# Performance work log

Hardware: AMD Instinct MI355X
Metric: run time of the kernel (lower is better)

## Reference

```python
import jax, jax.numpy as jnp
import numpy as np

EPS = 1e-08


def setup_inputs() -> dict:
    key = jax.random.key(0)
    x = jax.random.normal(key, (16384, 1024), dtype=jnp.float32)
    return {"x": x}


def reference(x) -> jnp.ndarray:
    # L2-normalize rows (torch F.normalize clamps the norm by eps=1e-12)
    norm = jnp.maximum(jnp.linalg.norm(x, axis=-1, keepdims=True), 1e-12)
    xn = x / norm
    # B x B cosine similarity
    sim = xn @ xn.T
    # exclude self-similarity on the diagonal
    B = sim.shape[0]
    diag = jnp.eye(B, dtype=bool)
    sim = jnp.where(diag, -jnp.inf, sim)
    max_sim = jnp.max(sim, axis=1)
    # squared L2 distance to nearest neighbor on the unit sphere
    distances = jnp.sqrt(2.0 - 2.0 * max_sim + EPS)
    return -jnp.mean(jnp.log(distances))
```

## Files before the change

kernel.cpp:

```cpp
#include <hip/hip_runtime.h>
#include <hip/hip_bf16.h>

#define NROWS 16384
#define DIM   1024
#define NT    8
#define NTILE 128
#define NBLK  (NTILE * (NTILE + 1) / 2)
#define SW    16

typedef int i32x4 __attribute__((ext_vector_type(4)));

__device__ __forceinline__ unsigned fkey(float f) {
    unsigned u = __float_as_uint(f);
    return (u & 0x80000000u) ? ~u : (u | 0x80000000u);
}
__device__ __forceinline__ float funkey(unsigned k) {
    unsigned u = (k & 0x80000000u) ? (k & 0x7fffffffu) : ~k;
    return __uint_as_float(u);
}

__global__ void normalize_rows(const float* __restrict__ x,
                               signed char* __restrict__ xq,
                               float* __restrict__ sinv,
                               unsigned* __restrict__ rowmax) {
    const int row = blockIdx.x;
    const int t = threadIdx.x;
    const float4 v = ((const float4*)(x + (size_t)row * DIM))[t];
    float ss = v.x * v.x + v.y * v.y + v.z * v.z + v.w * v.w;
#pragma unroll
    for (int off = 32; off > 0; off >>= 1) ss += __shfl_xor(ss, off);
    __shared__ float wss[4];
    __shared__ int   wqs[4];
    if ((t & 63) == 0) wss[t >> 6] = ss;
    __syncthreads();
    const float tot = wss[0] + wss[1] + wss[2] + wss[3];
    const float scale = 127.0f / fmaxf(sqrtf(tot), 1e-12f);
    int qx = __float2int_rn(v.x * scale);
    int qy = __float2int_rn(v.y * scale);
    int qz = __float2int_rn(v.z * scale);
    int qw = __float2int_rn(v.w * scale);
    qx = max(-127, min(127, qx)); qy = max(-127, min(127, qy));
    qz = max(-127, min(127, qz)); qw = max(-127, min(127, qw));
    const int p = (qx & 0xff) | ((qy & 0xff) << 8) | ((qz & 0xff) << 16) | ((qw & 0xff) << 24);
    ((int*)(xq + (size_t)row * DIM))[t] = p;
    int qs = qx * qx + qy * qy + qz * qz + qw * qw;
#pragma unroll
    for (int off = 32; off > 0; off >>= 1) qs += __shfl_xor(qs, off);
    if ((t & 63) == 0) wqs[t >> 6] = qs;
    __syncthreads();
    if (t == 0) {
        const int qtot = max(wqs[0] + wqs[1] + wqs[2] + wqs[3], 1);
        sinv[row] = 1.0f / sqrtf((float)qtot);
        rowmax[row] = 0u;
    }
}


#define SB() __builtin_amdgcn_sched_barrier(0)

__global__ __launch_bounds__(256, 2)
void simmax_kernel(const signed char* __restrict__ xq,
                   const float* __restrict__ sinv,
                   unsigned* __restrict__ rowmax) {
    const int bid = blockIdx.x;
    int rem = (bid & 7) * (NBLK / 8) + (bid >> 3);
    int s = 0;
    for (;;) {
        const int sz = 256 * s + 136;
        if (rem < sz) break;
        rem -= sz;
        ++s;
    }
    int it, jt;
    const int full = 256 * s;
    if (rem < full) {
        it = rem >> 4;
        jt = SW * s + (rem & 15);
    } else {
        int r2 = rem - full;
        int d = 0;
        while (r2 >= SW - d) { r2 -= SW - d; ++d; }
        it = SW * s + d;
        jt = it + r2;
    }
    const bool diag = (jt == it);
    const int rowBase = it * 128;
    const int colBase = jt * 128;

    __shared__ __align__(16) char lds[2][2][128][128];
    __shared__ unsigned redmax[256];

    const int t    = threadIdx.x;
    const int lane = t & 63;
    const int wid  = t >> 6;
    const int wr2  = wid >> 1;
    const int wc2  = wid & 1;
    const int l15  = lane & 15;
    const int hi   = lane >> 4;

    redmax[t] = 0u;

    const signed char* srcp[8];
#pragma unroll
    for (int j = 0; j < 8; ++j) {
        const int c   = j * 256 + t;
        const int op  = c >> 10;
        const int cc  = c & 1023;
        const int row = cc >> 3;
        const int ch  = cc & 7;
        const int gr  = (op ? colBase : rowBase) + row;
        srcp[j] = xq + (size_t)gr * DIM + (ch ^ (row & 7)) * 16;
    }

#pragma unroll
    for (int j = 0; j < 8; ++j) {
        __builtin_amdgcn_global_load_lds(
            (const __attribute__((address_space(1))) void*)srcp[j],
            (__attribute__((address_space(3))) void*)(&lds[0][0][0][0] + (j * 256 + wid * 64) * 16),
            16, 0, 0);
        srcp[j] += 128;
    }
    asm volatile("s_waitcnt vmcnt(0)" ::: "memory");
    __builtin_amdgcn_s_barrier();
    SB();

    i32x4 acc[4][4];
#pragma unroll
    for (int m = 0; m < 4; ++m)
#pragma unroll
        for (int n = 0; n < 4; ++n)
            acc[m][n] = (i32x4){0, 0, 0, 0};

    for (int tk = 0; tk < NT; ++tk) {
        char* curb = &lds[tk & 1][0][0][0];
        char* nxtb = &lds[(tk & 1) ^ 1][0][0][0];
        const bool pf = (tk + 1 < NT);

        i32x4 af[4][2], bf[4][2];
#pragma unroll
        for (int m = 0; m < 4; ++m)
#pragma unroll
            for (int kk = 0; kk < 2; ++kk) {
                const int row = wr2 * 64 + m * 16 + l15;
                const int chn = (kk * 4 + hi) ^ (row & 7);
                af[m][kk] = *(const i32x4*)(curb + row * 128 + chn * 16);
            }
        if (pf) {
#pragma unroll
            for (int j = 0; j < 4; ++j) {
                __builtin_amdgcn_global_load_lds(
                    (const __attribute__((address_space(1))) void*)srcp[j],
                    (__attribute__((address_space(3))) void*)(nxtb + (j * 256 + wid * 64) * 16),
                    16, 0, 0);
                srcp[j] += 128;
            }
        }
#pragma unroll
        for (int n = 0; n < 4; ++n)
#pragma unroll
            for (int kk = 0; kk < 2; ++kk) {
                const int row = wc2 * 64 + n * 16 + l15;
                const int chn = (kk * 4 + hi) ^ (row & 7);
                bf[n][kk] = *(const i32x4*)(curb + 16384 + row * 128 + chn * 16);
            }
        if (pf) {
#pragma unroll
            for (int j = 4; j < 8; ++j) {
                __builtin_amdgcn_global_load_lds(
                    (const __attribute__((address_space(1))) void*)srcp[j],
                    (__attribute__((address_space(3))) void*)(nxtb + (j * 256 + wid * 64) * 16),
                    16, 0, 0);
                srcp[j] += 128;
            }
        }
        __builtin_amdgcn_s_setprio(1);
#pragma unroll
        for (int m = 0; m < 4; ++m)
#pragma unroll
            for (int n = 0; n < 4; ++n)
#pragma unroll
                for (int kk = 0; kk < 2; ++kk)
                    acc[m][n] = __builtin_amdgcn_mfma_i32_16x16x64_i8(
                        af[m][kk], bf[n][kk], acc[m][n], 0, 0, 0);
        __builtin_amdgcn_s_setprio(0);

        asm volatile("s_waitcnt vmcnt(0)" ::: "memory");
        __builtin_amdgcn_s_barrier();
        SB();
    }

    const int g  = lane >> 4;
    const int cl = lane & 15;

    float scl_col[4];
#pragma unroll
    for (int n = 0; n < 4; ++n)
        scl_col[n] = sinv[colBase + wc2 * 64 + n * 16 + cl];
    float srow[4][4];
#pragma unroll
    for (int m = 0; m < 4; ++m)
#pragma unroll
        for (int r = 0; r < 4; ++r)
            srow[m][r] = sinv[rowBase + wr2 * 64 + m * 16 + g * 4 + r];

#pragma unroll
    for (int m = 0; m < 4; ++m)
#pragma unroll
        for (int r = 0; r < 4; ++r) {
            const int grow = wr2 * 64 + m * 16 + g * 4 + r;
            float v = -1e30f;
#pragma unroll
            for (int n = 0; n < 4; ++n) {
                const int gcol = wc2 * 64 + n * 16 + cl;
                float f = (float)acc[m][n][r] * scl_col[n];
                if (diag && grow == gcol) f = -1e30f;
                v = fmaxf(v, f);
            }
            v = fmaxf(v, __shfl_xor(v, 1));
            v = fmaxf(v, __shfl_xor(v, 2));
            v = fmaxf(v, __shfl_xor(v, 4));
            v = fmaxf(v, __shfl_xor(v, 8));
            if (cl == 0) atomicMax(&redmax[grow], fkey(v));
        }

    if (!diag) {
#pragma unroll
        for (int n = 0; n < 4; ++n) {
            float v = -1e30f;
#pragma unroll
            for (int m = 0; m < 4; ++m)
#pragma unroll
                for (int r = 0; r < 4; ++r)
                    v = fmaxf(v, (float)acc[m][n][r] * srow[m][r]);
            v = fmaxf(v, __shfl_xor(v, 16));
            v = fmaxf(v, __shfl_xor(v, 32));
            if (g == 0) atomicMax(&redmax[128 + wc2 * 64 + n * 16 + cl], fkey(v));
        }
    }
    __syncthreads();

    const unsigned k = redmax[t];
    if (t < 128) {
        atomicMax(rowmax + rowBase + t, k);
    } else if (!diag) {
        atomicMax(rowmax + colBase + (t - 128), k);
    }
}

__global__ void finalize_kernel(const unsigned* __restrict__ rowmax,
                                const float* __restrict__ sinv,
                                float* __restrict__ out) {
    const int t = threadIdx.x;
    float s = 0.f;
    for (int r = t; r < NROWS; r += 256) {
        const float m = fminf(sinv[r] * funkey(rowmax[r]), 1.0f);
        s += logf(2.0f - 2.0f * m + 1e-8f);
    }
#pragma unroll
    for (int off = 32; off > 0; off >>= 1) s += __shfl_xor(s, off);
    __shared__ float ws[4];
    if ((t & 63) == 0) ws[t >> 6] = s;
    __syncthreads();
    if (t == 0) out[0] = -0.5f * (ws[0] + ws[1] + ws[2] + ws[3]) / (float)NROWS;
}

extern "C" void kernel_launch(void* const* d_in, const int* in_sizes, int n_in,
                              void* d_out, int out_size, void* d_ws, size_t ws_size,
                              hipStream_t stream) {
    const float* x = (const float*)d_in[0];
    signed char* xq = (signed char*)d_ws;
    float* sinv = (float*)((char*)d_ws + (size_t)NROWS * DIM);
    unsigned* rowmax = (unsigned*)((char*)d_ws + (size_t)NROWS * DIM + NROWS * sizeof(float));
    float* out = (float*)d_out;

    normalize_rows<<<NROWS, 256, 0, stream>>>(x, xq, sinv, rowmax);
    simmax_kernel<<<NBLK, 256, 0, stream>>>(xq, sinv, rowmax);
    finalize_kernel<<<1, 256, 0, stream>>>(rowmax, sinv, out);
}
```

Before: 256.8 us.

## Load B operand directly from global into registers, halve LDS, raise occupancy

The B (column) tile is no longer staged through LDS. Each lane reads its MFMA B fragments straight from global memory, while only the A tile stays double-buffered in LDS. This halves LDS use per block, and launch bounds are raised to allow 4 blocks per CU, aiming to cut LDS traffic and improve latency hiding. The risk is that the direct B loads are uncoalesced, unswizzled and not prefetched, so MFMA may stall on global latency.

```diff
diff --git a/kernel.cpp b/kernel.cpp
--- a/kernel.cpp
+++ b/kernel.cpp
@@ -58,7 +58,7 @@
 
 #define SB() __builtin_amdgcn_sched_barrier(0)
 
-__global__ __launch_bounds__(256, 2)
+__global__ __launch_bounds__(256, 4)
 void simmax_kernel(const signed char* __restrict__ xq,
                    const float* __restrict__ sinv,
                    unsigned* __restrict__ rowmax) {
@@ -87,7 +87,7 @@
     const int rowBase = it * 128;
     const int colBase = jt * 128;
 
-    __shared__ __align__(16) char lds[2][2][128][128];
+    __shared__ __align__(16) char ldsA[2][16384];
     __shared__ unsigned redmax[256];
 
     const int t    = threadIdx.x;
@@ -100,25 +100,27 @@
 
     redmax[t] = 0u;
 
-    const signed char* srcp[8];
-#pragma unroll
-    for (int j = 0; j < 8; ++j) {
+    const signed char* srcA[4];
+#pragma unroll
+    for (int j = 0; j < 4; ++j) {
         const int c   = j * 256 + t;
-        const int op  = c >> 10;
-        const int cc  = c & 1023;
-        const int row = cc >> 3;
-        const int ch  = cc & 7;
-        const int gr  = (op ? colBase : rowBase) + row;
-        srcp[j] = xq + (size_t)gr * DIM + (ch ^ (row & 7)) * 16;
-    }
-
-#pragma unroll
-    for (int j = 0; j < 8; ++j) {
+        const int row = c >> 3;
+        const int ch  = c & 7;
+        srcA[j] = xq + (size_t)(rowBase + row) * DIM + (ch ^ (row & 7)) * 16;
+    }
+
+    const signed char* bn[4];
+#pragma unroll
+    for (int n = 0; n < 4; ++n)
+        bn[n] = xq + (size_t)(colBase + wc2 * 64 + n * 16 + l15) * DIM + hi * 16;
+
+#pragma unroll
+    for (int j = 0; j < 4; ++j) {
         __builtin_amdgcn_global_load_lds(
-            (const __attribute__((address_space(1))) void*)srcp[j],
-            (__attribute__((address_space(3))) void*)(&lds[0][0][0][0] + (j * 256 + wid * 64) * 16),
+            (const __attribute__((address_space(1))) void*)srcA[j],
+            (__attribute__((address_space(3))) void*)(&ldsA[0][0] + (j * 256 + wid * 64) * 16),
             16, 0, 0);
-        srcp[j] += 128;
+        srcA[j] += 128;
     }
     asm volatile("s_waitcnt vmcnt(0)" ::: "memory");
     __builtin_amdgcn_s_barrier();
@@ -132,47 +134,37 @@
             acc[m][n] = (i32x4){0, 0, 0, 0};
 
     for (int tk = 0; tk < NT; ++tk) {
-        char* curb = &lds[tk & 1][0][0][0];
-        char* nxtb = &lds[(tk & 1) ^ 1][0][0][0];
+        char* curA = &ldsA[tk & 1][0];
+        char* nxtA = &ldsA[(tk & 1) ^ 1][0];
         const bool pf = (tk + 1 < NT);
 
         i32x4 af[4][2], bf[4][2];
+#pragma unroll
+        for (int n = 0; n < 4; ++n)
+#pragma unroll
+            for (int kk = 0; kk < 2; ++kk)
+                bf[n][kk] = *(const i32x4*)(bn[n] + kk * 64);
 #pragma unroll
         for (int m = 0; m < 4; ++m)
 #pragma unroll
             for (int kk = 0; kk < 2; ++kk) {
                 const int row = wr2 * 64 + m * 16 + l15;
                 const int chn = (kk * 4 + hi) ^ (row & 7);
-                af[m][kk] = *(const i32x4*)(curb + row * 128 + chn * 16);
+                af[m][kk] = *(const i32x4*)(curA + row * 128 + chn * 16);
             }
         if (pf) {
 #pragma unroll
             for (int j = 0; j < 4; ++j) {
                 __builtin_amdgcn_global_load_lds(
-                    (const __attribute__((address_space(1))) void*)srcp[j],
-                    (__attribute__((address_space(3))) void*)(nxtb + (j * 256 + wid * 64) * 16),
+                    (const __attribute__((address_space(1))) void*)srcA[j],
+                    (__attribute__((address_space(3))) void*)(nxtA + (j * 256 + wid * 64) * 16),
                     16, 0, 0);
-                srcp[j] += 128;
+                srcA[j] += 128;
             }
         }
 #pragma unroll
-        for (int n = 0; n < 4; ++n)
-#pragma unroll
-            for (int kk = 0; kk < 2; ++kk) {
-                const int row = wc2 * 64 + n * 16 + l15;
-                const int chn = (kk * 4 + hi) ^ (row & 7);
-                bf[n][kk] = *(const i32x4*)(curb + 16384 + row * 128 + chn * 16);
-            }
-        if (pf) {
-#pragma unroll
-            for (int j = 4; j < 8; ++j) {
-                __builtin_amdgcn_global_load_lds(
-                    (const __attribute__((address_space(1))) void*)srcp[j],
-                    (__attribute__((address_space(3))) void*)(nxtb + (j * 256 + wid * 64) * 16),
-                    16, 0, 0);
-                srcp[j] += 128;
-            }
-        }
+        for (int n = 0; n < 4; ++n) bn[n] += 128;
+
         __builtin_amdgcn_s_setprio(1);
 #pragma unroll
         for (int m = 0; m < 4; ++m)
```

Result: slower. 700.4 us (+172.8%).
